# Optimization experiments

Measured on AMD Instinct MI355X. Metric: run time of the kernel, lower is better.

## Reference

```python
import jax, jax.numpy as jnp
import numpy as np

N_NODES = 50000
N_EDGES = 400000
IN_F, HID_F, OUT_F = 768, 16, 21


def setup_inputs() -> dict:
    key = jax.random.key(0)
    ks = jax.random.split(key, 7)
    feature = jax.random.normal(ks[0], (N_NODES, IN_F), dtype=jnp.float32)
    W1 = jax.random.normal(ks[1], (IN_F, HID_F), dtype=jnp.float32) * 0.03
    b1 = jax.random.normal(ks[2], (HID_F,), dtype=jnp.float32) * 0.01
    W2 = jax.random.normal(ks[3], (HID_F, OUT_F), dtype=jnp.float32) * 0.1
    b2 = jax.random.normal(ks[4], (OUT_F,), dtype=jnp.float32) * 0.01
    src = jax.random.randint(ks[5], (N_EDGES,), 0, N_NODES, dtype=jnp.int32)
    dst = jax.random.randint(ks[6], (N_EDGES,), 0, N_NODES, dtype=jnp.int32)
    return {"feature": feature, "W1": W1, "b1": b1, "W2": W2, "b2": b2,
            "src": src, "dst": dst}


def _gcn_agg(h, src, dst):
    # copy_src + sum reduce: gather source features along edges, scatter-add to dst
    return jax.ops.segment_sum(h[src], dst, num_segments=N_NODES)


def reference(feature, W1, b1, W2, b2, src, dst):
    # layer 1: aggregate then linear + relu
    h = _gcn_agg(feature, src, dst)            # [N, 768]
    h = jax.nn.relu(h @ W1 + b1)               # [N, 16]
    # layer 2: aggregate then linear (no activation)
    h = _gcn_agg(h, src, dst)                  # [N, 16]
    return h @ W2 + b2                         # [N, 21]
```

## Files before the change

kernel.cpp:

```cpp
#include <hip/hip_runtime.h>

#define NN 50000
#define NE 400000
#define INF 768
#define HF 16
#define OF 21
#define ELLW 40

#define FMA4(ACC, SS, VV) { (ACC).x += (SS)*(VV).x; (ACC).y += (SS)*(VV).y; \
                            (ACC).z += (SS)*(VV).z; (ACC).w += (SS)*(VV).w; }

__global__ __launch_bounds__(256) void scatter_kernel(const int* __restrict__ src,
                                                      const int* __restrict__ dst,
                                                      int* __restrict__ cnt,
                                                      int* __restrict__ ell) {
    int e = blockIdx.x * 256 + threadIdx.x;
    if (e >= NE) return;
    int d = dst[e];
    int pos = atomicAdd(&cnt[d], 1);
    if (pos < ELLW) ell[d * ELLW + pos] = src[e];
}

__global__ __launch_bounds__(512, 6) void gemm1_kernel(const float* __restrict__ F,
                                                       const float* __restrict__ W1,
                                                       float* __restrict__ P) {
    __shared__ float smem[INF * HF];

    const int t = threadIdx.x;
    {
        const float4* s = (const float4*)W1;
        float4* d = (float4*)smem;
        for (int i = t; i < (INF * HF) / 4; i += 512) d[i] = s[i];
    }
    __syncthreads();

    const int w = t >> 6, lane = t & 63;
    int row = blockIdx.x * 64 + lane;
    const bool act = row < NN;
    if (!act) row = NN - 1;

    const float4* fr = (const float4*)(F + (size_t)row * INF + w * 96);
    const float* wbase = smem + w * 96 * HF;

    float4 acc0 = {0,0,0,0}, acc1 = {0,0,0,0}, acc2 = {0,0,0,0}, acc3 = {0,0,0,0};
    float4 buf[8];
#pragma unroll
    for (int i = 0; i < 8; ++i) buf[i] = fr[i];

#pragma unroll
    for (int c = 0; c < 24; ++c) {
        float4 fv = buf[c & 7];
        if (c + 8 < 24) buf[c & 7] = fr[c + 8];
        const float* wr = wbase + c * 4 * HF;
#pragma unroll
        for (int m = 0; m < 4; ++m) {
            const float fm = (m == 0) ? fv.x : (m == 1) ? fv.y : (m == 2) ? fv.z : fv.w;
            const float4* wrow = (const float4*)(wr + m * HF);
            float4 w0 = wrow[0], w1 = wrow[1], w2 = wrow[2], w3 = wrow[3];
            FMA4(acc0, fm, w0);
            FMA4(acc1, fm, w1);
            FMA4(acc2, fm, w2);
            FMA4(acc3, fm, w3);
        }
    }

    __syncthreads();
    {
        float4* rp = (float4*)(smem + ((w * 64 + lane) << 4));
        rp[0] = acc0; rp[1] = acc1; rp[2] = acc2; rp[3] = acc3;
    }
    __syncthreads();

    if (t < 256) {
        const int r = t >> 2, q = t & 3;
        float4 s = {0,0,0,0};
#pragma unroll
        for (int ww = 0; ww < 8; ++ww) {
            float4 p = *(const float4*)(smem + ((ww * 64 + r) << 4) + q * 4);
            s.x += p.x; s.y += p.y; s.z += p.z; s.w += p.w;
        }
        const int orow = blockIdx.x * 64 + r;
        if (orow < NN)
            *(float4*)(P + (size_t)orow * HF + q * 4) = s;
    }
}

__global__ __launch_bounds__(256) void agg1_kernel(const float* __restrict__ P,
                                                   const int* __restrict__ cnt,
                                                   const int* __restrict__ ell,
                                                   float* __restrict__ A1) {
    int g = blockIdx.x * 256 + threadIdx.x;
    int node = g >> 4;
    if (node >= NN) return;
    const int l = g & 15, es = l >> 2, q = l & 3;
    int c = cnt[node]; if (c > ELLW) c = ELLW;
    const int* ep = ell + node * ELLW;

    float4 v = {0,0,0,0};
    for (int i = es; i < c; i += 4) {
        int s = ep[i];
        float4 p = *(const float4*)(P + (size_t)s * HF + q * 4);
        v.x += p.x; v.y += p.y; v.z += p.z; v.w += p.w;
    }
#define BFLY2(VAL) { VAL += __shfl_xor(VAL, 4); VAL += __shfl_xor(VAL, 8); }
    BFLY2(v.x) BFLY2(v.y) BFLY2(v.z) BFLY2(v.w)
#undef BFLY2
    if (es == 0)
        *(float4*)(A1 + (size_t)node * HF + q * 4) = v;
}

__global__ __launch_bounds__(256) void agg2out_kernel(const float* __restrict__ A1,
                                                      const float* __restrict__ b1,
                                                      const int* __restrict__ cnt,
                                                      const int* __restrict__ ell,
                                                      const float* __restrict__ W2,
                                                      const float* __restrict__ b2,
                                                      float* __restrict__ out) {
    __shared__ float W2s[HF * OF];
    __shared__ float b2s[OF];
    const int t = threadIdx.x;
    for (int i = t; i < HF * OF; i += 256) W2s[i] = W2[i];
    if (t < OF) b2s[t] = b2[t];
    __syncthreads();

    int g = blockIdx.x * 256 + t;
    int node = g >> 4;
    if (node >= NN) return;
    const int l = g & 15, es = l >> 2, q = l & 3;

    const float4 bb = *(const float4*)(b1 + q * 4);
    int c = cnt[node]; if (c > ELLW) c = ELLW;
    const int* ep = ell + node * ELLW;

    float4 v = {0,0,0,0};
    for (int i = es; i < c; i += 4) {
        int s = ep[i];
        float4 h = *(const float4*)(A1 + (size_t)s * HF + q * 4);
        h.x = fmaxf(h.x + bb.x, 0.0f);
        h.y = fmaxf(h.y + bb.y, 0.0f);
        h.z = fmaxf(h.z + bb.z, 0.0f);
        h.w = fmaxf(h.w + bb.w, 0.0f);
        v.x += h.x; v.y += h.y; v.z += h.z; v.w += h.w;
    }
#define BFLY2(VAL) { VAL += __shfl_xor(VAL, 4); VAL += __shfl_xor(VAL, 8); }
    BFLY2(v.x) BFLY2(v.y) BFLY2(v.z) BFLY2(v.w)
#undef BFLY2

    const float* w0 = W2s + (q * 4 + 0) * OF;
    const float* w1 = W2s + (q * 4 + 1) * OF;
    const float* w2 = W2s + (q * 4 + 2) * OF;
    const float* w3 = W2s + (q * 4 + 3) * OF;
    float o[OF];
#pragma unroll
    for (int cc = 0; cc < OF; ++cc)
        o[cc] = v.x * w0[cc] + v.y * w1[cc] + v.z * w2[cc] + v.w * w3[cc];
#pragma unroll
    for (int cc = 0; cc < OF; ++cc) {
        o[cc] += __shfl_xor(o[cc], 1);
        o[cc] += __shfl_xor(o[cc], 2);
    }
    if (es == 0) {
        float* op = out + (size_t)node * OF;
        for (int cc = q; cc < OF; cc += 4) op[cc] = o[cc] + b2s[cc];
    }
}

extern "C" void kernel_launch(void* const* d_in, const int* in_sizes, int n_in,
                              void* d_out, int out_size, void* d_ws, size_t ws_size,
                              hipStream_t stream) {
    const float* F   = (const float*)d_in[0];
    const float* W1  = (const float*)d_in[1];
    const float* b1  = (const float*)d_in[2];
    const float* W2  = (const float*)d_in[3];
    const float* b2  = (const float*)d_in[4];
    const int*   src = (const int*)d_in[5];
    const int*   dst = (const int*)d_in[6];
    float* out = (float*)d_out;

    char* ws = (char*)d_ws;
    int*   cnt = (int*)(ws);
    int*   ell = (int*)(ws + 200192);
    float* P   = (float*)(ws + 8200192);
    float* A1  = (float*)(ws + 11400192);

    (void)hipMemsetAsync(cnt, 0, NN * sizeof(int), stream);
    scatter_kernel<<<(NE + 255) / 256, 256, 0, stream>>>(src, dst, cnt, ell);
    gemm1_kernel<<<(NN + 63) / 64, 512, 0, stream>>>(F, W1, P);
    agg1_kernel<<<(NN * 16 + 255) / 256, 256, 0, stream>>>(P, cnt, ell, A1);
    agg2out_kernel<<<(NN * 16 + 255) / 256, 256, 0, stream>>>(A1, b1, cnt, ell, W2, b2, out);
}
```

Before: 313.4 us.

## Restructure feature GEMM to split K across lanes with shuffle reduction

The projection GEMM (F @ W1) now splits the 768-wide K dimension across the 16 lane-groups of a wavefront, each handling a float4 of columns over 8 rows. W1 is read straight from global/L1 and the LDS staging is dropped. Partial sums are combined with cross-lane shuffles instead of a shared-memory reduction across waves. The goal is more coalesced loads of the feature matrix and no LDS traffic or barriers, at the cost of redundant W1 loads and extra shuffle reductions per row.

```diff
diff --git a/kernel.cpp b/kernel.cpp
--- a/kernel.cpp
+++ b/kernel.cpp
@@ -21,67 +21,58 @@
     if (pos < ELLW) ell[d * ELLW + pos] = src[e];
 }
 
-__global__ __launch_bounds__(512, 6) void gemm1_kernel(const float* __restrict__ F,
+__global__ __launch_bounds__(256, 6) void gemm1_kernel(const float* __restrict__ F,
                                                        const float* __restrict__ W1,
                                                        float* __restrict__ P) {
-    __shared__ float smem[INF * HF];
+    const int tid = threadIdx.x;
+    const int wv = tid >> 6, lane = tid & 63;
+    const int g = lane >> 4;
+    const int u = lane & 15;
+    const int ks = u >> 2;
+    const int jq = u & 3;
+    const int koff = g * 16 + ks * 4;
+    const int rowbase = blockIdx.x * 32 + wv * 8;
 
-    const int t = threadIdx.x;
-    {
-        const float4* s = (const float4*)W1;
-        float4* d = (float4*)smem;
-        for (int i = t; i < (INF * HF) / 4; i += 512) d[i] = s[i];
+    int roff[8];
+#pragma unroll
+    for (int r = 0; r < 8; ++r) {
+        int row = rowbase + r;
+        if (row > NN - 1) row = NN - 1;
+        roff[r] = row * INF + koff;
     }
-    __syncthreads();
 
-    const int w = t >> 6, lane = t & 63;
-    int row = blockIdx.x * 64 + lane;
-    const bool act = row < NN;
-    if (!act) row = NN - 1;
+    const float* wbase = W1 + koff * HF + jq * 4;
 
-    const float4* fr = (const float4*)(F + (size_t)row * INF + w * 96);
-    const float* wbase = smem + w * 96 * HF;
+    float4 acc[8];
+#pragma unroll
+    for (int r = 0; r < 8; ++r) acc[r] = make_float4(0.f, 0.f, 0.f, 0.f);
 
-    float4 acc0 = {0,0,0,0}, acc1 = {0,0,0,0}, acc2 = {0,0,0,0}, acc3 = {0,0,0,0};
-    float4 buf[8];
+    for (int t = 0; t < INF / 64; ++t) {
+        const float* wp = wbase + t * 64 * HF;
+        const float4 w0 = *(const float4*)(wp + 0 * HF);
+        const float4 w1 = *(const float4*)(wp + 1 * HF);
+        const float4 w2 = *(const float4*)(wp + 2 * HF);
+        const float4 w3 = *(const float4*)(wp + 3 * HF);
 #pragma unroll
-    for (int i = 0; i < 8; ++i) buf[i] = fr[i];
-
-#pragma unroll
-    for (int c = 0; c < 24; ++c) {
-        float4 fv = buf[c & 7];
-        if (c + 8 < 24) buf[c & 7] = fr[c + 8];
-        const float* wr = wbase + c * 4 * HF;
-#pragma unroll
-        for (int m = 0; m < 4; ++m) {
-            const float fm = (m == 0) ? fv.x : (m == 1) ? fv.y : (m == 2) ? fv.z : fv.w;
-            const float4* wrow = (const float4*)(wr + m * HF);
-            float4 w0 = wrow[0], w1 = wrow[1], w2 = wrow[2], w3 = wrow[3];
-            FMA4(acc0, fm, w0);
-            FMA4(acc1, fm, w1);
-            FMA4(acc2, fm, w2);
-            FMA4(acc3, fm, w3);
+        for (int r = 0; r < 8; ++r) {
+            const float4 f = *(const float4*)(F + roff[r] + t * 64);
+            FMA4(acc[r], f.x, w0);
+            FMA4(acc[r], f.y, w1);
+            FMA4(acc[r], f.z, w2);
+            FMA4(acc[r], f.w, w3);
         }
     }
 
-    __syncthreads();
-    {
-        float4* rp = (float4*)(smem + ((w * 64 + lane) << 4));
-        rp[0] = acc0; rp[1] = acc1; rp[2] = acc2; rp[3] = acc3;
-    }
-    __syncthreads();
-
-    if (t < 256) {
-        const int r = t >> 2, q = t & 3;
-        float4 s = {0,0,0,0};
 #pragma unroll
-        for (int ww = 0; ww < 8; ++ww) {
-            float4 p = *(const float4*)(smem + ((ww * 64 + r) << 4) + q * 4);
-            s.x += p.x; s.y += p.y; s.z += p.z; s.w += p.w;
-        }
-        const int orow = blockIdx.x * 64 + r;
-        if (orow < NN)
-            *(float4*)(P + (size_t)orow * HF + q * 4) = s;
+    for (int r = 0; r < 8; ++r) {
+        float4 v = acc[r];
+#define RED(X) { v.X += __shfl_xor(v.X, 4);  v.X += __shfl_xor(v.X, 8); \
+                 v.X += __shfl_xor(v.X, 16); v.X += __shfl_xor(v.X, 32); }
+        RED(x) RED(y) RED(z) RED(w)
+#undef RED
+        const int row = rowbase + r;
+        if (lane < 4 && row < NN)
+            *(float4*)(P + (size_t)row * HF + jq * 4) = v;
     }
 }
 
@@ -185,7 +176,7 @@
 
     (void)hipMemsetAsync(cnt, 0, NN * sizeof(int), stream);
     scatter_kernel<<<(NE + 255) / 256, 256, 0, stream>>>(src, dst, cnt, ell);
-    gemm1_kernel<<<(NN + 63) / 64, 512, 0, stream>>>(F, W1, P);
+    gemm1_kernel<<<(NN + 31) / 32, 256, 0, stream>>>(F, W1, P);
     agg1_kernel<<<(NN * 16 + 255) / 256, 256, 0, stream>>>(P, cnt, ell, A1);
     agg2out_kernel<<<(NN * 16 + 255) / 256, 256, 0, stream>>>(A1, b1, cnt, ell, W2, b2, out);
 }
```

Measured after the change: 401.1 us. 1.28x slower.
